# Optimization experiments

Measured on AMD Instinct MI355X. Metric: run time of the kernel, lower is better.

Reference implementation:

```python
import jax, jax.numpy as jnp
import numpy as np

B, F, Q = 8192, 128, 64
H1, H2 = 256, 256
THRESHOLD = 0.95
EPS = 1e-12


def setup_inputs() -> dict:
    key = jax.random.key(0)
    ks = jax.random.split(key, 8)
    in_dim = F + 1 + Q  # raw + quantum + graph feature
    def lin(k, fan_in, fan_out):
        bound = 1.0 / np.sqrt(fan_in)
        kw, kb = jax.random.split(k)
        W = jax.random.uniform(kw, (fan_out, fan_in), jnp.float32, -bound, bound)
        b = jax.random.uniform(kb, (fan_out,), jnp.float32, -bound, bound)
        return W, b
    W1, b1 = lin(ks[2], in_dim, H1)
    W2, b2 = lin(ks[3], H1, H2)
    W3, b3 = lin(ks[4], H2, 1)
    return {
        'x': jax.random.normal(ks[0], (B, F), jnp.float32),
        'quantum_features': jax.random.normal(ks[1], (B, Q), jnp.float32),
        'W1': W1, 'b1': b1, 'W2': W2, 'b2': b2, 'W3': W3, 'b3': b3,
    }


def _graph_feat(x):
    # normalized Gram matrix -> squared cosine fidelity -> threshold -> row mean
    xn = x / (jnp.linalg.norm(x, axis=1, keepdims=True) + EPS)  # [B, F]
    fid = jnp.square(xn @ xn.T)                                  # [B, B]
    adj = jnp.where(fid >= THRESHOLD, 1.0, 0.0)
    adj = adj * (1.0 - jnp.eye(x.shape[0], dtype=x.dtype))       # no self-edges
    return jnp.mean(adj, axis=1, keepdims=True)                  # [B, 1]


def reference(x, quantum_features, W1, b1, W2, b2, W3, b3):
    graph_feat = jax.lax.stop_gradient(_graph_feat(x))  # built under no_grad in torch
    feats = jnp.concatenate([x, quantum_features, graph_feat], axis=1)  # [B, F+Q+1]
    h = jax.nn.relu(feats @ W1.T + b1)
    h = jax.nn.relu(h @ W2.T + b2)
    out = h @ W3.T + b3  # [B, 1]
    return out[:, 0]
```

## Files before the change

### kernel.cpp

```cpp
#include <hip/hip_runtime.h>
#include <hip/hip_bf16.h>

typedef __attribute__((ext_vector_type(8))) short bf16x8;
typedef __attribute__((ext_vector_type(8))) int i32x8;
typedef __attribute__((ext_vector_type(4))) float f32x4;
typedef unsigned int uint;

#define NROWS 8192
#define F_DIM 128
#define Q_DIM 64
#define KPAD  224
#define H_DIM 256

static __device__ inline unsigned short bf_bits(__hip_bfloat16 b) {
  unsigned short u; __builtin_memcpy(&u, &b, 2); return u;
}
static __device__ inline uint packhl(float v) {
  __hip_bfloat16 h = __float2bfloat16(v);
  float hf = __bfloat162float(h);
  __hip_bfloat16 l = __float2bfloat16(v - hf);
  return ((uint)bf_bits(l) << 16) | (uint)bf_bits(h);
}
static __device__ inline void split_hl(float v, unsigned short& h, unsigned short& l) {
  __hip_bfloat16 hb = __float2bfloat16(v);
  float hf = __bfloat162float(hb);
  __hip_bfloat16 lb = __float2bfloat16(v - hf);
  h = bf_bits(hb); l = bf_bits(lb);
}

union uu { uint4 u; bf16x8 v; };

__global__ __launch_bounds__(256) void norm_prep_kernel(const float* __restrict__ x,
                                                        const float* __restrict__ W1,
                                                        const float* __restrict__ W2,
                                                        unsigned char* __restrict__ xn8,
                                                        uint* __restrict__ W1P,
                                                        uint* __restrict__ W2P,
                                                        int* __restrict__ cnt) {
  int tid = threadIdx.x;
  int bid = blockIdx.x;
  if (bid < 256) {
    W2P[bid * 256 + tid] = packhl(W2[bid * 256 + tid]);
  } else if (bid < 512) {
    int n = bid - 256;
    if (tid < KPAD) W1P[n * KPAD + tid] = (tid < 193) ? packhl(W1[n * 193 + tid]) : 0u;
  }
  if (bid < 32) cnt[bid * 256 + tid] = 0;

  int lane = tid & 63;
  int row = bid * 4 + (tid >> 6);
  const float2 v = *(const float2*)(x + (size_t)row * F_DIM + lane * 2);
  float s = v.x * v.x + v.y * v.y;
#pragma unroll
  for (int off = 32; off; off >>= 1) s += __shfl_xor(s, off);
  float inv = 1.0f / (sqrtf(s) + 1e-12f);
  int pk = __builtin_amdgcn_cvt_pk_fp8_f32(v.x * inv, v.y * inv, 0, 0);
  *(unsigned short*)(xn8 + (size_t)row * F_DIM + lane * 2) = (unsigned short)(pk & 0xffff);
}

__global__ __launch_bounds__(256) void gram8_kernel(const unsigned char* __restrict__ xn8,
                                                    int* __restrict__ cnt) {
  __shared__ char smem[32768];
  int tid = threadIdx.x;
  int lane = tid & 63;
  int wave = tid >> 6;
  int lr = lane & 15;
  int quad = lane >> 4;

  int t = blockIdx.x;
  int bi = (int)((129.0f - sqrtf(129.0f * 129.0f - 8.0f * (float)t)) * 0.5f);
  while ((bi + 1) * (129 - (bi + 1)) / 2 <= t) bi++;
  while (bi * (129 - bi) / 2 > t) bi--;
  int bj = bi + (t - bi * (129 - bi) / 2);
  int i0 = bi * 128, j0 = bj * 128;

#pragma unroll
  for (int it = 0; it < 8; ++it) {
    int half = it >> 2;
    int row = (it & 3) * 32 + (tid >> 3);
    int chunk = tid & 7;
    int grow = (half ? j0 : i0) + row;
    uint4 v = *(const uint4*)(xn8 + (size_t)grow * F_DIM + chunk * 16);
    *(uint4*)(smem + half * 16384 + row * 128 + ((chunk ^ (row & 7)) << 4)) = v;
  }
  __syncthreads();

  int wi = (wave >> 1) * 64, wj = (wave & 1) * 64;

  f32x4 acc[4][4];
#pragma unroll
  for (int i = 0; i < 4; i++)
#pragma unroll
    for (int j = 0; j < 4; j++) acc[i][j] = (f32x4){0.f, 0.f, 0.f, 0.f};

  i32x8 a[4], b[4];
#pragma unroll
  for (int tt = 0; tt < 4; tt++) {
    int r = wi + tt * 16 + lr;
    const char* base = smem + r * 128;
    uint4 lo = *(const uint4*)(base + (((2 * quad) ^ (r & 7)) << 4));
    uint4 hi = *(const uint4*)(base + (((2 * quad + 1) ^ (r & 7)) << 4));
    i32x8 f;
    f[0] = lo.x; f[1] = lo.y; f[2] = lo.z; f[3] = lo.w;
    f[4] = hi.x; f[5] = hi.y; f[6] = hi.z; f[7] = hi.w;
    a[tt] = f;
  }
#pragma unroll
  for (int tt = 0; tt < 4; tt++) {
    int r = wj + tt * 16 + lr;
    const char* base = smem + 16384 + r * 128;
    uint4 lo = *(const uint4*)(base + (((2 * quad) ^ (r & 7)) << 4));
    uint4 hi = *(const uint4*)(base + (((2 * quad + 1) ^ (r & 7)) << 4));
    i32x8 f;
    f[0] = lo.x; f[1] = lo.y; f[2] = lo.z; f[3] = lo.w;
    f[4] = hi.x; f[5] = hi.y; f[6] = hi.z; f[7] = hi.w;
    b[tt] = f;
  }

#pragma unroll
  for (int tr = 0; tr < 4; tr++)
#pragma unroll
    for (int tc = 0; tc < 4; tc++)
      acc[tr][tc] = __builtin_amdgcn_mfma_scale_f32_16x16x128_f8f6f4(
          a[tr], b[tc], acc[tr][tc], 0, 0, 0, 0x7f7f7f7f, 0, 0x7f7f7f7f);

  int i_base = i0 + wi, j_base = j0 + wj;
  bool diag_wave = (i_base == j_base);
  bool offdiag_block = (bi != bj);

  float mx = 0.f;
#pragma unroll
  for (int tr = 0; tr < 4; tr++)
#pragma unroll
    for (int tc = 0; tc < 4; tc++)
#pragma unroll
      for (int r = 0; r < 4; r++) {
        float v = acc[tr][tc][r];
        if (diag_wave && tr == tc && lr == quad * 4 + r) v = 0.f;
        mx = fmaxf(mx, fabsf(v));
      }
  if (__any(mx >= 0.9746f)) {
    for (int tr = 0; tr < 4; tr++)
      for (int tc = 0; tc < 4; tc++)
        for (int r = 0; r < 4; r++) {
          float v = acc[tr][tc][r];
          int row = i_base + tr * 16 + quad * 4 + r;
          int col = j_base + tc * 16 + lr;
          if (v * v >= 0.95f && row != col) {
            atomicAdd(&cnt[row], 1);
            if (offdiag_block) atomicAdd(&cnt[col], 1);
          }
        }
  }
}

__global__ __launch_bounds__(256) void fused_mlp_kernel(const float* __restrict__ x,
                                                        const float* __restrict__ q,
                                                        const uint* __restrict__ W1P,
                                                        const uint* __restrict__ W2P,
                                                        const float* __restrict__ b1,
                                                        const float* __restrict__ b2,
                                                        const float* __restrict__ W3,
                                                        const float* __restrict__ b3,
                                                        const int* __restrict__ cnt,
                                                        float* __restrict__ out) {
  __shared__ char smem[65536];
  short* Ahs = (short*)smem;
  short* Als = (short*)(smem + 14848);
  uint*  H1  = (uint*)smem;
  uint*  Bx  = (uint*)(smem + 32768);
  float* part = (float*)(smem + 32768);

  int tid = threadIdx.x;
  int lane = tid & 63;
  int wv = tid >> 6;
  int lr = lane & 15;
  int quad = lane >> 4;
  int mb = blockIdx.x * 32;

  {
    int r = tid >> 3;
    int c8 = (tid & 7) * 4;
#pragma unroll
    for (int it = 0; it < 7; ++it) {
      int col = it * 32 + c8;
      float4 v = {0.f, 0.f, 0.f, 0.f};
      if (it < 4)      v = *(const float4*)(x + (size_t)(mb + r) * F_DIM + col);
      else if (it < 6) v = *(const float4*)(q + (size_t)(mb + r) * Q_DIM + (col - 128));
      else if (c8 == 0) v.x = (float)cnt[mb + r] * (1.0f / 8192.0f);
      unsigned short h0, l0, h1, l1, h2, l2, h3, l3;
      split_hl(v.x, h0, l0); split_hl(v.y, h1, l1);
      split_hl(v.z, h2, l2); split_hl(v.w, h3, l3);
      *(uint2*)&Ahs[r * 232 + col] = (uint2){(uint)h0 | ((uint)h1 << 16), (uint)h2 | ((uint)h3 << 16)};
      *(uint2*)&Als[r * 232 + col] = (uint2){(uint)l0 | ((uint)l1 << 16), (uint)l2 | ((uint)l3 << 16)};
    }
  }

  f32x4 acc[2][4];
#pragma unroll
  for (int i = 0; i < 2; i++)
#pragma unroll
    for (int j = 0; j < 4; j++) acc[i][j] = (f32x4){0.f, 0.f, 0.f, 0.f};

  for (int kc = 0; kc < 7; ++kc) {
    int k0 = kc * 32;
    __syncthreads();
#pragma unroll
    for (int i = 0; i < 8; ++i) {
      int flat = i * 256 + tid;
      int n = flat >> 3, j = flat & 7;
      uint4 w = *(const uint4*)(W1P + (size_t)n * KPAD + k0 + j * 4);
      *(uint4*)&Bx[n * 32 + ((j ^ (n & 7)) * 4)] = w;
    }
    __syncthreads();
    bf16x8 ah[2], al[2], bh[4], bl[4];
#pragma unroll
    for (int tt = 0; tt < 2; ++tt) {
      int row = tt * 16 + lr;
      ah[tt] = *(const bf16x8*)&Ahs[row * 232 + k0 + quad * 8];
      al[tt] = *(const bf16x8*)&Als[row * 232 + k0 + quad * 8];
    }
#pragma unroll
    for (int tc = 0; tc < 4; ++tc) {
      int n = wv * 64 + tc * 16 + lr;
      uint4 u0 = *(const uint4*)&Bx[n * 32 + (((quad * 2) ^ (n & 7)) * 4)];
      uint4 u1 = *(const uint4*)&Bx[n * 32 + (((quad * 2 + 1) ^ (n & 7)) * 4)];
      uu h, l;
      h.u.x = (u0.x & 0xffffu) | (u0.y << 16);
      h.u.y = (u0.z & 0xffffu) | (u0.w << 16);
      h.u.z = (u1.x & 0xffffu) | (u1.y << 16);
      h.u.w = (u1.z & 0xffffu) | (u1.w << 16);
      l.u.x = (u0.x >> 16) | (u0.y & 0xffff0000u);
      l.u.y = (u0.z >> 16) | (u0.w & 0xffff0000u);
      l.u.z = (u1.x >> 16) | (u1.y & 0xffff0000u);
      l.u.w = (u1.z >> 16) | (u1.w & 0xffff0000u);
      bh[tc] = h.v; bl[tc] = l.v;
    }
#pragma unroll
    for (int tt = 0; tt < 2; ++tt)
#pragma unroll
      for (int tc = 0; tc < 4; ++tc) {
        acc[tt][tc] = __builtin_amdgcn_mfma_f32_16x16x32_bf16(ah[tt], bh[tc], acc[tt][tc], 0, 0, 0);
        acc[tt][tc] = __builtin_amdgcn_mfma_f32_16x16x32_bf16(ah[tt], bl[tc], acc[tt][tc], 0, 0, 0);
        acc[tt][tc] = __builtin_amdgcn_mfma_f32_16x16x32_bf16(al[tt], bh[tc], acc[tt][tc], 0, 0, 0);
      }
  }

  __syncthreads();
#pragma unroll
  for (int tc = 0; tc < 4; ++tc) {
    int n = wv * 64 + tc * 16 + lr;
    float bv = b1[n];
    int g = n >> 2, jj = n & 3;
#pragma unroll
    for (int tt = 0; tt < 2; ++tt)
#pragma unroll
      for (int r = 0; r < 4; ++r) {
        int row = tt * 16 + quad * 4 + r;
        float v = fmaxf(acc[tt][tc][r] + bv, 0.f);
        H1[row * 256 + ((g ^ (row & 31)) * 4 + jj)] = packhl(v);
      }
  }
#pragma unroll
  for (int i = 0; i < 2; i++)
#pragma unroll
    for (int j = 0; j < 4; j++) acc[i][j] = (f32x4){0.f, 0.f, 0.f, 0.f};

  for (int kc = 0; kc < 8; ++kc) {
    int k0 = kc * 32;
    __syncthreads();
#pragma unroll
    for (int i = 0; i < 8; ++i) {
      int flat = i * 256 + tid;
      int n = flat >> 3, j = flat & 7;
      uint4 w = *(const uint4*)(W2P + (size_t)n * 256 + k0 + j * 4);
      *(uint4*)&Bx[n * 32 + ((j ^ (n & 7)) * 4)] = w;
    }
    __syncthreads();
    bf16x8 ah[2], al[2], bh[4], bl[4];
#pragma unroll
    for (int tt = 0; tt < 2; ++tt) {
      int row = tt * 16 + lr;
      int cb = kc * 8 + quad * 2;
      uint4 u0 = *(const uint4*)&H1[row * 256 + ((cb ^ (row & 31)) * 4)];
      uint4 u1 = *(const uint4*)&H1[row * 256 + (((cb + 1) ^ (row & 31)) * 4)];
      uu h, l;
      h.u.x = (u0.x & 0xffffu) | (u0.y << 16);
      h.u.y = (u0.z & 0xffffu) | (u0.w << 16);
      h.u.z = (u1.x & 0xffffu) | (u1.y << 16);
      h.u.w = (u1.z & 0xffffu) | (u1.w << 16);
      l.u.x = (u0.x >> 16) | (u0.y & 0xffff0000u);
      l.u.y = (u0.z >> 16) | (u0.w & 0xffff0000u);
      l.u.z = (u1.x >> 16) | (u1.y & 0xffff0000u);
      l.u.w = (u1.z >> 16) | (u1.w & 0xffff0000u);
      ah[tt] = h.v; al[tt] = l.v;
    }
#pragma unroll
    for (int tc = 0; tc < 4; ++tc) {
      int n = wv * 64 + tc * 16 + lr;
      uint4 u0 = *(const uint4*)&Bx[n * 32 + (((quad * 2) ^ (n & 7)) * 4)];
      uint4 u1 = *(const uint4*)&Bx[n * 32 + (((quad * 2 + 1) ^ (n & 7)) * 4)];
      uu h, l;
      h.u.x = (u0.x & 0xffffu) | (u0.y << 16);
      h.u.y = (u0.z & 0xffffu) | (u0.w << 16);
      h.u.z = (u1.x & 0xffffu) | (u1.y << 16);
      h.u.w = (u1.z & 0xffffu) | (u1.w << 16);
      l.u.x = (u0.x >> 16) | (u0.y & 0xffff0000u);
      l.u.y = (u0.z >> 16) | (u0.w & 0xffff0000u);
      l.u.z = (u1.x >> 16) | (u1.y & 0xffff0000u);
      l.u.w = (u1.z >> 16) | (u1.w & 0xffff0000u);
      bh[tc] = h.v; bl[tc] = l.v;
    }
#pragma unroll
    for (int tt = 0; tt < 2; ++tt)
#pragma unroll
      for (int tc = 0; tc < 4; ++tc) {
        acc[tt][tc] = __builtin_amdgcn_mfma_f32_16x16x32_bf16(ah[tt], bh[tc], acc[tt][tc], 0, 0, 0);
        acc[tt][tc] = __builtin_amdgcn_mfma_f32_16x16x32_bf16(ah[tt], bl[tc], acc[tt][tc], 0, 0, 0);
        acc[tt][tc] = __builtin_amdgcn_mfma_f32_16x16x32_bf16(al[tt], bh[tc], acc[tt][tc], 0, 0, 0);
      }
  }

  float s[2][4];
#pragma unroll
  for (int tt = 0; tt < 2; ++tt)
#pragma unroll
    for (int r = 0; r < 4; ++r) s[tt][r] = 0.f;
#pragma unroll
  for (int tc = 0; tc < 4; ++tc) {
    int n = wv * 64 + tc * 16 + lr;
    float bv = b2[n];
    float w3 = W3[n];
#pragma unroll
    for (int tt = 0; tt < 2; ++tt)
#pragma unroll
      for (int r = 0; r < 4; ++r)
        s[tt][r] += fmaxf(acc[tt][tc][r] + bv, 0.f) * w3;
  }
#pragma unroll
  for (int tt = 0; tt < 2; ++tt)
#pragma unroll
    for (int r = 0; r < 4; ++r) {
      s[tt][r] += __shfl_xor(s[tt][r], 1);
      s[tt][r] += __shfl_xor(s[tt][r], 2);
      s[tt][r] += __shfl_xor(s[tt][r], 4);
      s[tt][r] += __shfl_xor(s[tt][r], 8);
    }
  __syncthreads();
  if (lr == 0) {
#pragma unroll
    for (int tt = 0; tt < 2; ++tt)
#pragma unroll
      for (int r = 0; r < 4; ++r)
        part[wv * 32 + tt * 16 + quad * 4 + r] = s[tt][r];
  }
  __syncthreads();
  if (tid < 32)
    out[mb + tid] = part[tid] + part[32 + tid] + part[64 + tid] + part[96 + tid] + b3[0];
}

extern "C" void kernel_launch(void* const* d_in, const int* in_sizes, int n_in,
                              void* d_out, int out_size, void* d_ws, size_t ws_size,
                              hipStream_t stream) {
  const float* x  = (const float*)d_in[0];
  const float* q  = (const float*)d_in[1];
  const float* W1 = (const float*)d_in[2];
  const float* b1 = (const float*)d_in[3];
  const float* W2 = (const float*)d_in[4];
  const float* b2 = (const float*)d_in[5];
  const float* W3 = (const float*)d_in[6];
  const float* b3 = (const float*)d_in[7];
  float* out = (float*)d_out;

  char* ws = (char*)d_ws;
  unsigned char* xn8 = (unsigned char*)(ws);
  int*  cnt = (int*)(ws + 0x100000);
  uint* W1P = (uint*)(ws + 0x110000);
  uint* W2P = (uint*)(ws + 0x150000);

  norm_prep_kernel<<<dim3(2048), dim3(256), 0, stream>>>(x, W1, W2, xn8, W1P, W2P, cnt);
  gram8_kernel<<<dim3(2080), dim3(256), 0, stream>>>(xn8, cnt);
  fused_mlp_kernel<<<dim3(256), dim3(256), 0, stream>>>(x, q, W1P, W2P, b1, b2, W3, b3, cnt, out);
}
```

Before: 97.93 us.

## Read MLP weights directly from global as split hi/lo bf16 planes

Weight preprocessing now stores separate hi and lo bf16 arrays instead of interleaved packed words. The MLP kernel loads B fragments straight from global/L2 instead of staging them through LDS with barriers and repacking shifts. The graph-feature column is removed from the K dimension and added as a rank-1 FP32 update after layer one, cutting K from 224 to 192. This drops per-chunk syncthreads and LDS traffic, but relies on L2/L1 to serve redundant weight loads across waves.

```diff
diff --git a/kernel.cpp b/kernel.cpp
--- a/kernel.cpp
+++ b/kernel.cpp
@@ -5,12 +5,14 @@
 typedef __attribute__((ext_vector_type(8))) int i32x8;
 typedef __attribute__((ext_vector_type(4))) float f32x4;
 typedef unsigned int uint;
+typedef unsigned short u16;
 
 #define NROWS 8192
 #define F_DIM 128
 #define Q_DIM 64
-#define KPAD  224
+#define K1    192
 #define H_DIM 256
+#define APITCH 200
 
 static __device__ inline unsigned short bf_bits(__hip_bfloat16 b) {
   unsigned short u; __builtin_memcpy(&u, &b, 2); return u;
@@ -34,16 +36,25 @@
                                                         const float* __restrict__ W1,
                                                         const float* __restrict__ W2,
                                                         unsigned char* __restrict__ xn8,
-                                                        uint* __restrict__ W1P,
-                                                        uint* __restrict__ W2P,
+                                                        u16* __restrict__ W1h, u16* __restrict__ W1l,
+                                                        u16* __restrict__ W2h, u16* __restrict__ W2l,
+                                                        float* __restrict__ W1g,
                                                         int* __restrict__ cnt) {
   int tid = threadIdx.x;
   int bid = blockIdx.x;
   if (bid < 256) {
-    W2P[bid * 256 + tid] = packhl(W2[bid * 256 + tid]);
+    u16 h, l; split_hl(W2[bid * 256 + tid], h, l);
+    W2h[bid * 256 + tid] = h;
+    W2l[bid * 256 + tid] = l;
   } else if (bid < 512) {
     int n = bid - 256;
-    if (tid < KPAD) W1P[n * KPAD + tid] = (tid < 193) ? packhl(W1[n * 193 + tid]) : 0u;
+    if (tid < K1) {
+      u16 h, l; split_hl(W1[n * 193 + tid], h, l);
+      W1h[n * K1 + tid] = h;
+      W1l[n * K1 + tid] = l;
+    } else if (tid == K1) {
+      W1g[n] = W1[n * 193 + 192];
+    }
   }
   if (bid < 32) cnt[bid * 256 + tid] = 0;
 
@@ -156,20 +167,22 @@
 
 __global__ __launch_bounds__(256) void fused_mlp_kernel(const float* __restrict__ x,
                                                         const float* __restrict__ q,
-                                                        const uint* __restrict__ W1P,
-                                                        const uint* __restrict__ W2P,
+                                                        const u16* __restrict__ W1h,
+                                                        const u16* __restrict__ W1l,
+                                                        const u16* __restrict__ W2h,
+                                                        const u16* __restrict__ W2l,
+                                                        const float* __restrict__ W1g,
                                                         const float* __restrict__ b1,
                                                         const float* __restrict__ b2,
                                                         const float* __restrict__ W3,
                                                         const float* __restrict__ b3,
                                                         const int* __restrict__ cnt,
                                                         float* __restrict__ out) {
-  __shared__ char smem[65536];
+  __shared__ __align__(16) char smem[58368];
   short* Ahs = (short*)smem;
-  short* Als = (short*)(smem + 14848);
-  uint*  H1  = (uint*)smem;
-  uint*  Bx  = (uint*)(smem + 32768);
-  float* part = (float*)(smem + 32768);
+  short* Als = (short*)(smem + 12800);
+  uint*  H1  = (uint*)(smem + 25600);
+  float* part = (float*)smem;
 
   int tid = threadIdx.x;
   int lane = tid & 63;
@@ -182,19 +195,19 @@
     int r = tid >> 3;
     int c8 = (tid & 7) * 4;
 #pragma unroll
-    for (int it = 0; it < 7; ++it) {
+    for (int it = 0; it < 6; ++it) {
       int col = it * 32 + c8;
-      float4 v = {0.f, 0.f, 0.f, 0.f};
-      if (it < 4)      v = *(const float4*)(x + (size_t)(mb + r) * F_DIM + col);
-      else if (it < 6) v = *(const float4*)(q + (size_t)(mb + r) * Q_DIM + (col - 128));
-      else if (c8 == 0) v.x = (float)cnt[mb + r] * (1.0f / 8192.0f);
+      float4 v;
+      if (it < 4) v = *(const float4*)(x + (size_t)(mb + r) * F_DIM + col);
+      else        v = *(const float4*)(q + (size_t)(mb + r) * Q_DIM + (col - 128));
       unsigned short h0, l0, h1, l1, h2, l2, h3, l3;
       split_hl(v.x, h0, l0); split_hl(v.y, h1, l1);
       split_hl(v.z, h2, l2); split_hl(v.w, h3, l3);
-      *(uint2*)&Ahs[r * 232 + col] = (uint2){(uint)h0 | ((uint)h1 << 16), (uint)h2 | ((uint)h3 << 16)};
-      *(uint2*)&Als[r * 232 + col] = (uint2){(uint)l0 | ((uint)l1 << 16), (uint)l2 | ((uint)l3 << 16)};
-    }
-  }
+      *(uint2*)&Ahs[r * APITCH + col] = (uint2){(uint)h0 | ((uint)h1 << 16), (uint)h2 | ((uint)h3 << 16)};
+      *(uint2*)&Als[r * APITCH + col] = (uint2){(uint)l0 | ((uint)l1 << 16), (uint)l2 | ((uint)l3 << 16)};
+    }
+  }
+  __syncthreads();
 
   f32x4 acc[2][4];
 #pragma unroll
@@ -202,39 +215,20 @@
 #pragma unroll
     for (int j = 0; j < 4; j++) acc[i][j] = (f32x4){0.f, 0.f, 0.f, 0.f};
 
-  for (int kc = 0; kc < 7; ++kc) {
+  for (int kc = 0; kc < 6; ++kc) {
     int k0 = kc * 32;
-    __syncthreads();
-#pragma unroll
-    for (int i = 0; i < 8; ++i) {
-      int flat = i * 256 + tid;
-      int n = flat >> 3, j = flat & 7;
-      uint4 w = *(const uint4*)(W1P + (size_t)n * KPAD + k0 + j * 4);
-      *(uint4*)&Bx[n * 32 + ((j ^ (n & 7)) * 4)] = w;
-    }
-    __syncthreads();
     bf16x8 ah[2], al[2], bh[4], bl[4];
 #pragma unroll
     for (int tt = 0; tt < 2; ++tt) {
       int row = tt * 16 + lr;
-      ah[tt] = *(const bf16x8*)&Ahs[row * 232 + k0 + quad * 8];
-      al[tt] = *(const bf16x8*)&Als[row * 232 + k0 + quad * 8];
+      ah[tt] = *(const bf16x8*)&Ahs[row * APITCH + k0 + quad * 8];
+      al[tt] = *(const bf16x8*)&Als[row * APITCH + k0 + quad * 8];
     }
 #pragma unroll
     for (int tc = 0; tc < 4; ++tc) {
       int n = wv * 64 + tc * 16 + lr;
-      uint4 u0 = *(const uint4*)&Bx[n * 32 + (((quad * 2) ^ (n & 7)) * 4)];
-      uint4 u1 = *(const uint4*)&Bx[n * 32 + (((quad * 2 + 1) ^ (n & 7)) * 4)];
-      uu h, l;
-      h.u.x = (u0.x & 0xffffu) | (u0.y << 16);
-      h.u.y = (u0.z & 0xffffu) | (u0.w << 16);
-      h.u.z = (u1.x & 0xffffu) | (u1.y << 16);
-      h.u.w = (u1.z & 0xffffu) | (u1.w << 16);
-      l.u.x = (u0.x >> 16) | (u0.y & 0xffff0000u);
-      l.u.y = (u0.z >> 16) | (u0.w & 0xffff0000u);
-      l.u.z = (u1.x >> 16) | (u1.y & 0xffff0000u);
-      l.u.w = (u1.z >> 16) | (u1.w & 0xffff0000u);
-      bh[tc] = h.v; bl[tc] = l.v;
+      bh[tc] = *(const bf16x8*)(W1h + (size_t)n * K1 + k0 + quad * 8);
+      bl[tc] = *(const bf16x8*)(W1l + (size_t)n * K1 + k0 + quad * 8);
     }
 #pragma unroll
     for (int tt = 0; tt < 2; ++tt)
@@ -246,7 +240,25 @@
       }
   }
 
-  __syncthreads();
+  {
+    float gv[2][4];
+#pragma unroll
+    for (int tt = 0; tt < 2; ++tt)
+#pragma unroll
+      for (int r = 0; r < 4; ++r)
+        gv[tt][r] = (float)cnt[mb + tt * 16 + quad * 4 + r] * (1.0f / 8192.0f);
+#pragma unroll
+    for (int tc = 0; tc < 4; ++tc) {
+      int n = wv * 64 + tc * 16 + lr;
+      float w = W1g[n];
+#pragma unroll
+      for (int tt = 0; tt < 2; ++tt)
+#pragma unroll
+        for (int r = 0; r < 4; ++r)
+          acc[tt][tc][r] += gv[tt][r] * w;
+    }
+  }
+
 #pragma unroll
   for (int tc = 0; tc < 4; ++tc) {
     int n = wv * 64 + tc * 16 + lr;
@@ -265,18 +277,9 @@
   for (int i = 0; i < 2; i++)
 #pragma unroll
     for (int j = 0; j < 4; j++) acc[i][j] = (f32x4){0.f, 0.f, 0.f, 0.f};
+  __syncthreads();
 
   for (int kc = 0; kc < 8; ++kc) {
-    int k0 = kc * 32;
-    __syncthreads();
-#pragma unroll
-    for (int i = 0; i < 8; ++i) {
-      int flat = i * 256 + tid;
-      int n = flat >> 3, j = flat & 7;
-      uint4 w = *(const uint4*)(W2P + (size_t)n * 256 + k0 + j * 4);
-      *(uint4*)&Bx[n * 32 + ((j ^ (n & 7)) * 4)] = w;
-    }
-    __syncthreads();
     bf16x8 ah[2], al[2], bh[4], bl[4];
 #pragma unroll
     for (int tt = 0; tt < 2; ++tt) {
@@ -298,18 +301,8 @@
 #pragma unroll
     for (int tc = 0; tc < 4; ++tc) {
       int n = wv * 64 + tc * 16 + lr;
-      uint4 u0 = *(const uint4*)&Bx[n * 32 + (((quad * 2) ^ (n & 7)) * 4)];
-      uint4 u1 = *(const uint4*)&Bx[n * 32 + (((quad * 2 + 1) ^ (n & 7)) * 4)];
-      uu h, l;
-      h.u.x = (u0.x & 0xffffu) | (u0.y << 16);
-      h.u.y = (u0.z & 0xffffu) | (u0.w << 16);
-      h.u.z = (u1.x & 0xffffu) | (u1.y << 16);
-      h.u.w = (u1.z & 0xffffu) | (u1.w << 16);
-      l.u.x = (u0.x >> 16) | (u0.y & 0xffff0000u);
-      l.u.y = (u0.z >> 16) | (u0.w & 0xffff0000u);
-      l.u.z = (u1.x >> 16) | (u1.y & 0xffff0000u);
-      l.u.w = (u1.z >> 16) | (u1.w & 0xffff0000u);
-      bh[tc] = h.v; bl[tc] = l.v;
+      bh[tc] = *(const bf16x8*)(W2h + (size_t)n * 256 + kc * 32 + quad * 8);
+      bl[tc] = *(const bf16x8*)(W2l + (size_t)n * 256 + kc * 32 + quad * 8);
     }
 #pragma unroll
     for (int tt = 0; tt < 2; ++tt)
@@ -346,7 +339,6 @@
       s[tt][r] += __shfl_xor(s[tt][r], 4);
       s[tt][r] += __shfl_xor(s[tt][r], 8);
     }
-  __syncthreads();
   if (lr == 0) {
 #pragma unroll
     for (int tt = 0; tt < 2; ++tt)
@@ -374,11 +366,14 @@
 
   char* ws = (char*)d_ws;
   unsigned char* xn8 = (unsigned char*)(ws);
-  int*  cnt = (int*)(ws + 0x100000);
-  uint* W1P = (uint*)(ws + 0x110000);
-  uint* W2P = (uint*)(ws + 0x150000);
-
-  norm_prep_kernel<<<dim3(2048), dim3(256), 0, stream>>>(x, W1, W2, xn8, W1P, W2P, cnt);
+  int*   cnt = (int*)(ws + 0x100000);
+  u16*   W1h = (u16*)(ws + 0x110000);
+  u16*   W1l = (u16*)(ws + 0x128000);
+  u16*   W2h = (u16*)(ws + 0x140000);
+  u16*   W2l = (u16*)(ws + 0x160000);
+  float* W1g = (float*)(ws + 0x180000);
+
+  norm_prep_kernel<<<dim3(2048), dim3(256), 0, stream>>>(x, W1, W2, xn8, W1h, W1l, W2h, W2l, W1g, cnt);
   gram8_kernel<<<dim3(2080), dim3(256), 0, stream>>>(xn8, cnt);
-  fused_mlp_kernel<<<dim3(256), dim3(256), 0, stream>>>(x, q, W1P, W2P, b1, b2, W3, b3, cnt, out);
-}
+  fused_mlp_kernel<<<dim3(256), dim3(256), 0, stream>>>(x, q, W1h, W1l, W2h, W2l, W1g, b1, b2, W3, b3, cnt, out);
+}
```

New measurement: 95.23 us. -2.8%, faster.
